# Performance work log

Measured on AMD Instinct MI355X. Metric: run time of the kernel, lower is better.

Reference implementation:

```python
import jax, jax.numpy as jnp
import numpy as np

# ---- static model dims (from init_kwargs) ----
M = 128          # latent_seq_length
Mp1 = M + 1
K = 2 * Mp1      # HMM states (m,g): m in 0..M, g in {0: match, 1: insert}; k = m + (M+1)*g
D = 21           # alphabet_length
ZD = 64          # z_dim
B = 64           # batch size
L = 256          # obs_seq_length
P = Mp1 * 3 * 2  # flattened indel-parameter count (M+1, 3, 2)
NEG = -1e32      # -1/epsilon (pyro Profile epsilon=1e-32) -> forbidden transitions


def _cell_factors(n0, g, mp, gp):
    """Indel log-prob factors (param indices (m,j,s)) for a transition into state (mp,gp)
    when the next undecided ancestral slot is n0 and source type is j=g.
    j: 0=from match, 1=from insert, 2=after deletion. s: 0=no indel, 1=indel.
    Returns (insert_factors, delete_factors) or None if the transition is forbidden."""
    if mp < n0:
        return None
    rs, us = [], []
    if mp == n0:
        if gp == 0:
            rs.append((n0, g, 0)); us.append((n0, g, 0))
        else:
            rs.append((n0, g, 1))
    else:
        rs.append((n0, g, 0)); us.append((n0, g, 1))
        for mm in range(n0 + 1, mp):
            rs.append((mm, 2, 0)); us.append((mm, 2, 1))
        if gp == 0:
            rs.append((mp, 2, 0)); us.append((mp, 2, 0))
        else:
            rs.append((mp, 2, 1))
    return rs, us


def _build_tables():
    k_of = lambda m, g: m + Mp1 * g
    p_of = lambda m, j, s: (m * 3 + j) * 2 + s
    # initial-distribution transfer (dense, small): virtual source (m,g)=(-1,0) -> n0=0
    r0 = np.zeros((P, K), np.float32)
    u0 = np.zeros((P, K), np.float32)
    null0 = np.zeros((K,), np.float32)
    for mp in range(Mp1):
        for gp in range(2):
            f = _cell_factors(0, 0, mp, gp)
            kp = k_of(mp, gp)
            if f is None:
                null0[kp] = 1.0
            else:
                for t in f[0]:
                    r0[p_of(*t), kp] += 1.0
                for t in f[1]:
                    u0[p_of(*t), kp] += 1.0
    # transition-matrix transfer: sparse (param_idx, cell_idx) scatter-add lists
    r_par, r_cell, u_par, u_cell = [], [], [], []
    null = np.zeros((K, K), np.float32)
    for m in range(Mp1):
        for g in range(2):
            n0, k = m + 1 - g, k_of(m, g)
            for mp in range(Mp1):
                for gp in range(2):
                    kp = k_of(mp, gp)
                    f = _cell_factors(n0, g, mp, gp)
                    if f is None:
                        null[k, kp] = 1.0
                    else:
                        cell = k * K + kp
                        for t in f[0]:
                            r_par.append(p_of(*t)); r_cell.append(cell)
                        for t in f[1]:
                            u_par.append(p_of(*t)); u_cell.append(cell)
    return (jnp.asarray(r0), jnp.asarray(u0), jnp.asarray(null0), jnp.asarray(null),
            jnp.asarray(np.asarray(r_par, np.int32)), jnp.asarray(np.asarray(r_cell, np.int32)),
            jnp.asarray(np.asarray(u_par, np.int32)), jnp.asarray(np.asarray(u_cell, np.int32)))


R0, U0, NULL0, NULL, R_PAR, R_CELL, U_PAR, U_CELL = _build_tables()


def setup_inputs() -> dict:
    key = jax.random.key(0)
    ks = jax.random.split(key, 8)
    # variable-length one-hot sequences; missing steps are all-zero rows (pyro convention)
    tokens = jax.random.randint(ks[0], (B, L), 0, D)
    lengths = jax.random.randint(ks[1], (B,), L // 2, L + 1)
    mask = jnp.arange(L)[None, :] < lengths[:, None]
    data = jax.nn.one_hot(tokens, D, dtype=jnp.float32) * mask[:, :, None]
    z = jax.random.normal(ks[2], (B, ZD), jnp.float32)
    out_dim = 2 * Mp1 * D
    dec_W = jax.random.normal(ks[3], (out_dim, ZD), jnp.float32) / np.sqrt(ZD).astype(np.float32)
    dec_b = jax.random.normal(ks[4], (out_dim,), jnp.float32) * 0.01
    indel_prior = jnp.array([10.0, 0.0], jnp.float32)  # [strength, 0]
    insert = indel_prior + jax.random.normal(ks[5], (Mp1, 3, 2), jnp.float32)
    delete = indel_prior + jax.random.normal(ks[6], (Mp1, 3, 2), jnp.float32)
    inverse_temp = 1.0 + 0.1 * jax.random.normal(ks[7], (1,), jnp.float32)
    return {"data": data, "z": z, "dec_W": dec_W, "dec_b": dec_b,
            "insert": insert, "delete": delete, "inverse_temp": inverse_temp}


def reference(data, z, dec_W, dec_b, insert, delete, inverse_temp):
    # ---- Decoder + temperature-sharpened emission logits (FactorMuE.model) ----
    latent = (z @ dec_W.T + dec_b).reshape(-1, 2, Mp1, D)        # (B, 2, M+1, D)
    it = jax.nn.softplus(inverse_temp[0])
    anc = latent[:, 0] * it
    anc = anc - jax.nn.logsumexp(anc, axis=-1, keepdims=True)    # ancestor_seq_logits
    insq = latent[:, 1] * it
    insq = insq - jax.nn.logsumexp(insq, axis=-1, keepdims=True)  # insert_seq_logits
    ilog = insert - jax.nn.logsumexp(insert, axis=-1, keepdims=True)
    dlog = delete - jax.nn.logsumexp(delete, axis=-1, keepdims=True)
    # ---- Profile state arranger: profile-HMM -> dense HMM logits ----
    pi, pd = ilog.reshape(-1), dlog.reshape(-1)                  # (P,)
    a0 = pd @ U0 + pi @ R0 + NEG * NULL0                         # (K,) initial logits
    a = (jnp.zeros((K * K,), pi.dtype)
         .at[U_CELL].add(pd[U_PAR])
         .at[R_CELL].add(pi[R_PAR])).reshape(K, K) + NEG * NULL  # (K, K) transition logits
    e = jnp.concatenate([anc, insq], axis=1)                     # (B, K, D), k = m + (M+1)*g
    # ---- VariableLengthDiscreteHMM (MissingDataDiscreteHMM) log_prob ----
    a0 = a0 - jax.nn.logsumexp(a0)
    a = a - jax.nn.logsumexp(a, axis=-1, keepdims=True)
    e = e - jax.nn.logsumexp(e, axis=-1, keepdims=True)
    vl = jnp.einsum('bld,bkd->lbk', data, e)                     # (L, B, K); zero rows -> 0 (missing)
    alpha = a0 + vl[0]                                           # (B, K)

    def step(alpha, v):
        alpha = jax.nn.logsumexp(alpha[:, :, None] + a[None], axis=1) + v
        return alpha, None

    alpha, _ = jax.lax.scan(step, alpha, vl[1:])
    return jax.nn.logsumexp(alpha, axis=-1)                      # (B,) log-likelihood per sequence
```

## Files before the change

### kernel.cpp

```cpp
#include <hip/hip_runtime.h>
#include <math.h>

#define MP1 129
#define KK  258
#define DD  21
#define ZDIM 64
#define BB  64
#define LL  256

#define OFF_ETG  0
#define OFF_E2G  360448
#define OFF_TOK  363264
#define OFF_COEF 379648
#define C_UU   0
#define C_DXM  258
#define C_DXI  516
#define C_WM   774
#define C_WI   903
#define C_DMID 1032
#define C_PI0  1160

#define EMIS_BLKS 65
#define TOK_BLKS  1366

typedef float f32x2 __attribute__((ext_vector_type(2)));

template <int CTRL, int RM, int BM>
__device__ __forceinline__ float updpp(float old, float src) {
    return __int_as_float(__builtin_amdgcn_update_dpp(
        __float_as_int(old), __float_as_int(src), CTRL, RM, BM, false));
}
__device__ __forceinline__ float readlane_f(float v, int lane) {
    return __int_as_float(__builtin_amdgcn_readlane(__float_as_int(v), lane));
}
__device__ __forceinline__ float wave_sum_to63(float s) {
    s += updpp<0x111, 0xf, 0xf>(0.f, s);
    s += updpp<0x112, 0xf, 0xf>(0.f, s);
    s += updpp<0x114, 0xf, 0xf>(0.f, s);
    s += updpp<0x118, 0xf, 0xf>(0.f, s);
    s += updpp<0x142, 0xa, 0xf>(0.f, s);
    s += updpp<0x143, 0xc, 0xf>(0.f, s);
    return s;
}

__global__ __launch_bounds__(256, 1) void k_setup(const float* __restrict__ z,
                                                  const float* __restrict__ W,
                                                  const float* __restrict__ bias,
                                                  const float* __restrict__ invt,
                                                  const float* __restrict__ data,
                                                  const float* __restrict__ ins,
                                                  const float* __restrict__ del,
                                                  float* __restrict__ ETg,
                                                  float* __restrict__ E2g,
                                                  int* __restrict__ tokout,
                                                  float* __restrict__ coef) {
    __shared__ float il[774], dl[774], Smid[129], Qs[130];
    int bid = blockIdx.x;
    int tid = threadIdx.x;

    if (bid >= 1 && bid <= EMIS_BLKS) {
        int b  = tid & 63;
        int rr = __builtin_amdgcn_readfirstlane((bid - 1) * 4 + (tid >> 6));
        if (rr >= KK) return;
        float it = log1pf(expf(invt[0]));
        const float* wb = W + (size_t)rr * DD * ZDIM;
        const float* bp = bias + rr * DD;
        float acc[DD];
        #pragma unroll
        for (int d = 0; d < DD; ++d) acc[d] = bp[d];
        const float4* zp = (const float4*)(z + (size_t)b * ZDIM);
        #pragma unroll
        for (int c = 0; c < 4; ++c) {
            float4 za = zp[4 * c + 0], zb = zp[4 * c + 1];
            float4 zc = zp[4 * c + 2], zd = zp[4 * c + 3];
            #pragma unroll
            for (int d = 0; d < DD; ++d) {
                const float4* wp = (const float4*)(wb + (size_t)d * ZDIM + 16 * c);
                float4 wa = wp[0], wv = wp[1], wc = wp[2], wd = wp[3];
                float a = acc[d];
                a = fmaf(za.x, wa.x, a); a = fmaf(za.y, wa.y, a);
                a = fmaf(za.z, wa.z, a); a = fmaf(za.w, wa.w, a);
                a = fmaf(zb.x, wv.x, a); a = fmaf(zb.y, wv.y, a);
                a = fmaf(zb.z, wv.z, a); a = fmaf(zb.w, wv.w, a);
                a = fmaf(zc.x, wc.x, a); a = fmaf(zc.y, wc.y, a);
                a = fmaf(zc.z, wc.z, a); a = fmaf(zc.w, wc.w, a);
                a = fmaf(zd.x, wd.x, a); a = fmaf(zd.y, wd.y, a);
                a = fmaf(zd.z, wd.z, a); a = fmaf(zd.w, wd.w, a);
                acc[d] = a;
            }
        }
        float mx = acc[0] * it;
        #pragma unroll
        for (int d = 0; d < DD; ++d) { acc[d] *= it; mx = fmaxf(mx, acc[d]); }
        float s = 0.f;
        #pragma unroll
        for (int d = 0; d < DD; ++d) { acc[d] = expf(acc[d] - mx); s += acc[d]; }
        float inv = 1.0f / s;
        if (rr == 128 || rr == 257) {
            float* eb = E2g + b * 44 + ((rr == 128) ? 0 : 1);
            #pragma unroll
            for (int d = 0; d < DD; ++d) eb[d * 2] = acc[d] * inv;
            eb[DD * 2] = 1.0f;
        } else {
            bool ism = rr < 128;
            int m = ism ? rr : rr - MP1;
            int slot = (m >> 1) * 4 + (ism ? 0 : 2) + (m & 1);
            float* eb = ETg + (size_t)b * 5632 + slot;
            #pragma unroll
            for (int d = 0; d < DD; ++d) eb[d * 256] = acc[d] * inv;
            eb[DD * 256] = 1.0f;
        }
        return;
    }
    if (bid > EMIS_BLKS) {
        int wid  = (bid - 1 - EMIS_BLKS) * 4 + (tid >> 6);
        int lane = tid & 63;
        int r3   = lane / 21;
        int d    = lane - r3 * 21;
        int row  = wid * 3 + r3;
        float v = 0.f;
        if (r3 < 3 && row < BB * LL) v = data[(size_t)row * DD + d];
        unsigned long long m = __ballot(v > 0.5f);
        if (r3 < 3 && d == 0 && row < BB * LL) {
            unsigned long long slice = (m >> (21 * r3)) & 0x1FFFFFULL;
            tokout[row] = slice ? (int)__builtin_ctzll(slice) : DD;
        }
        return;
    }
    int t = tid;
    for (int p = t; p < 387; p += 256) {
        float x0 = ins[2 * p], x1 = ins[2 * p + 1];
        float mx = fmaxf(x0, x1);
        float ls = mx + logf(expf(x0 - mx) + expf(x1 - mx));
        il[2 * p] = x0 - ls; il[2 * p + 1] = x1 - ls;
        float y0 = del[2 * p], y1 = del[2 * p + 1];
        float my = fmaxf(y0, y1);
        float lt = my + logf(expf(y0 - my) + expf(y1 - my));
        dl[2 * p] = y0 - lt; dl[2 * p + 1] = y1 - lt;
    }
    __syncthreads();
    if (t < 64) {
        int mmA = 1 + 2 * t, mmB = 2 + 2 * t;
        float xA = il[(mmA * 3 + 2) * 2 + 0] + dl[(mmA * 3 + 2) * 2 + 1];
        float xB = il[(mmB * 3 + 2) * 2 + 0] + dl[(mmB * 3 + 2) * 2 + 1];
        float sc = xA + xB;
        #pragma unroll
        for (int off = 1; off < 64; off <<= 1) {
            float vv = __shfl_up(sc, off);
            if (t >= off) sc += vv;
        }
        Smid[mmB] = sc;
        Smid[mmA] = sc - xB;
        if (t == 0) Smid[0] = 0.f;
    }
    __syncthreads();
    if (t < 64) {
        int mpA = 128 - 2 * t, mpB = 127 - 2 * t;
        float aM_ = il[(mpA * 3 + 2) * 2 + 0] + dl[(mpA * 3 + 2) * 2 + 0];
        float aI_ = il[(mpA * 3 + 2) * 2 + 1];
        float mA = fmaxf(aM_, aI_);
        float pA = Smid[mpA - 1] + mA + logf(expf(aM_ - mA) + expf(aI_ - mA));
        float bM_ = il[(mpB * 3 + 2) * 2 + 0] + dl[(mpB * 3 + 2) * 2 + 0];
        float bI_ = il[(mpB * 3 + 2) * 2 + 1];
        float mB = fmaxf(bM_, bI_);
        float pB = Smid[mpB - 1] + mB + logf(expf(bM_ - mB) + expf(bI_ - mB));
        float cm = fmaxf(pA, pB);
        float cs = expf(pA - cm) + expf(pB - cm);
        #pragma unroll
        for (int off = 1; off < 64; off <<= 1) {
            float om = __shfl_up(cm, off);
            float os = __shfl_up(cs, off);
            if (t >= off) {
                float M = fmaxf(cm, om);
                cs = cs * expf(cm - M) + os * expf(om - M);
                cm = M;
            }
        }
        Qs[mpB] = cm + logf(cs);
        float em = __shfl_up(cm, 1), es = __shfl_up(cs, 1);
        if (t == 0) Qs[128] = pA;
        else {
            float M = fmaxf(em, pA);
            Qs[mpA] = M + logf(es * expf(em - M) + expf(pA - M));
        }
        if (t == 0) Qs[129] = -1e30f;
    }
    __syncthreads();
    float* uu  = coef + C_UU;
    float* dxM = coef + C_DXM;
    float* dxI = coef + C_DXI;
    float* wM  = coef + C_WM;
    float* wI  = coef + C_WI;
    float* dmd = coef + C_DMID;
    float* pi0 = coef + C_PI0;
    for (int k = t; k < KK; k += 256) {
        if (k == 128) { uu[k] = 0.f; dxM[k] = 0.f; dxI[k] = 0.f; continue; }
        int g  = (k < MP1) ? 0 : 1;
        int n0 = g ? (k - MP1) : (k + 1);
        float i0 = il[(n0 * 3 + g) * 2 + 0], i1 = il[(n0 * 3 + g) * 2 + 1];
        float e0 = dl[(n0 * 3 + g) * 2 + 0], e1 = dl[(n0 * 3 + g) * 2 + 1];
        float diagM = i0 + e0;
        float diagI = i1;
        float src   = i0 + e1;
        float tail  = src - Smid[n0] + Qs[n0 + 1];
        float M3 = fmaxf(fmaxf(diagM, diagI), tail);
        float ssum = expf(diagM - M3) + expf(diagI - M3) + expf(tail - M3);
        float lse = M3 + logf(ssum);
        uu[k]  = expf(src - lse);
        dxM[k] = expf(diagM - lse);
        dxI[k] = expf(diagI - lse);
    }
    for (int mp = t; mp < MP1; mp += 256) {
        wM[mp] = expf(il[(mp * 3 + 2) * 2 + 0] + dl[(mp * 3 + 2) * 2 + 0]);
        wI[mp] = expf(il[(mp * 3 + 2) * 2 + 1]);
    }
    for (int tt = t; tt < 128; tt += 256)
        dmd[tt] = (tt == 0) ? 1.f : expf(il[(tt * 3 + 2) * 2 + 0] + dl[(tt * 3 + 2) * 2 + 1]);
    __syncthreads();
    {
        float i00 = il[0], i01 = il[1], d00 = dl[0], d01 = dl[1];
        float a00 = i00 + d00, a0129 = i01;
        float tail0 = i00 + d01 + Qs[1];
        float M3 = fmaxf(fmaxf(a00, a0129), tail0);
        float lse0 = M3 + logf(expf(a00 - M3) + expf(a0129 - M3) + expf(tail0 - M3));
        for (int kp = t; kp < KK; kp += 256) {
            int gp = (kp >= MP1);
            int mp = gp ? (kp - MP1) : kp;
            float v;
            if (mp == 0) v = gp ? a0129 : a00;
            else v = i00 + d01 + Smid[mp - 1] +
                     (gp ? il[(mp * 3 + 2) * 2 + 1]
                         : il[(mp * 3 + 2) * 2 + 0] + dl[(mp * 3 + 2) * 2 + 0]);
            pi0[kp] = expf(v - lse0);
        }
    }
}

__global__ __launch_bounds__(64) void k_fwd(const float* __restrict__ ETg,
                                            const float* __restrict__ E2g,
                                            const int* __restrict__ tokg,
                                            const float* __restrict__ coef,
                                            float* __restrict__ out) {
    const float* uu  = coef + C_UU;
    const float* dxM = coef + C_DXM;
    const float* dxI = coef + C_DXI;
    const float* wMg = coef + C_WM;
    const float* wIg = coef + C_WI;
    const float* dmd = coef + C_DMID;
    const float* pi0 = coef + C_PI0;
    __shared__ float ETLs[22 * 256];
    int lane = threadIdx.x;
    int b = blockIdx.x;
    const float4* srcp = (const float4*)(ETg + (size_t)b * 5632);
    float4* dstp = (float4*)ETLs;
    for (int i = lane; i < 1408; i += 64) dstp[i] = srcp[i];
    float e2m = 0.f, e2i = 0.f;
    if (lane < 22) {
        e2m = E2g[b * 44 + lane * 2 + 0];
        e2i = E2g[b * 44 + lane * 2 + 1];
    }
    int4 tkv = ((const int4*)(tokg + b * LL))[lane];
    __syncthreads();

    int m0 = 2 * lane, m1 = 2 * lane + 1;
    bool L0 = (lane == 0), L63 = (lane == 63);
    float f63 = L63 ? 1.f : 0.f;
    float cM0 = L0 ? 0.f : uu[m0 - 1];
    float cM1 = uu[m0];
    f32x2 cIp  = {uu[129 + m0], uu[129 + m1]};
    float d0 = dmd[m0], d1v = dmd[m1];
    float Apair = d0 * d1v;
    f32x2 wMp  = {wMg[m0], wMg[m1]};
    f32x2 wIp  = {wIg[m0], wIg[m1]};
    f32x2 xMAp = {L0 ? 0.f : dxM[m0 - 1], dxM[m0]};
    f32x2 xIAp = {L0 ? 0.f : dxI[m0 - 1], dxI[m0]};
    f32x2 xMBp = {dxM[129 + m0], dxM[129 + m1]};
    f32x2 xIBp = {dxI[129 + m0], dxI[129 + m1]};
    f32x2 w2p  = {L63 ? wMg[128] : 0.f, L63 ? wIg[128] : 0.f};
    f32x2 xA2p = {L63 ? dxM[127] : 0.f, L63 ? dxI[127] : 0.f};
    f32x2 xB2p = {L63 ? dxM[257] : 0.f, L63 ? dxI[257] : 0.f};
    f32x2 f63p = {f63, f63};

    float A0 = Apair;
    float A1 = A0 * updpp<0x111, 0xf, 0xf>(1.f, A0);
    float A2 = A1 * updpp<0x112, 0xf, 0xf>(1.f, A1);
    float A3 = A2 * updpp<0x114, 0xf, 0xf>(1.f, A2);
    float A4 = A3 * updpp<0x118, 0xf, 0xf>(1.f, A3);
    float A5 = A4 * updpp<0x142, 0xa, 0xf>(1.f, A4);
    unsigned long long bbf = __ballot(Apair >= 1.0e-3f);
    int fast = (bbf == 0ULL);

    int lidx = lane * 4;
    int tok0 = __builtin_amdgcn_readlane(tkv.x, 0);
    float4 q0 = *(const float4*)(ETLs + tok0 * 256 + lidx);
    f32x2 e20 = {readlane_f(e2m, tok0), readlane_f(e2i, tok0)};
    f32x2 aM = {pi0[m0] * q0.x, pi0[m1] * q0.y};
    f32x2 aI = {pi0[129 + m0] * q0.z, pi0[129 + m1] * q0.w};
    f32x2 a2 = {f63 * pi0[128] * e20.x, f63 * pi0[257] * e20.y};

    int etot = 0;
    f32x2 part = (aM + aI) + a2;

    float4 q1, q2, q3, q4;
    int st1, st2, st3, st4;
#define LOADR(QN, SN, TN)                                                    \
    { int tn_ = (TN); SN = tn_;                                              \
      QN = *(const float4*)(ETLs + tn_ * 256 + lidx); }
    LOADR(q1, st1, __builtin_amdgcn_readlane(tkv.y, 0));
    LOADR(q2, st2, __builtin_amdgcn_readlane(tkv.z, 0));
    LOADR(q3, st3, __builtin_amdgcn_readlane(tkv.w, 0));
    LOADR(q4, st4, __builtin_amdgcn_readlane(tkv.x, 1));

#define STEP_BODY(RES, PART, NL, Qr, STr)                                    \
    {                                                                        \
        f32x2 EMv = {Qr.x, Qr.y};                                            \
        f32x2 EIv = {Qr.z, Qr.w};                                            \
        f32x2 E2v = {readlane_f(e2m, STr), readlane_f(e2i, STr)};            \
        if (RES) {                                                           \
            float s_ = wave_sum_to63(part.x + part.y);                       \
            float stot = readlane_f(s_, 63);                                 \
            int sb = __float_as_int(stot) & 0x7f800000;                      \
            etot += (sb >> 23);                                              \
            float invs = __int_as_float(0x7f000000 - sb);                    \
            f32x2 iv = {invs, invs};                                         \
            EMv *= iv; EIv *= iv; E2v *= iv;                                 \
        }                                                                    \
        float aMp  = updpp<0x138, 0xf, 0xf>(0.f, aM.y);        \
        float u128 = readlane_f(a2.x, 63);                                   \
        f32x2 aIc = aI * cIp;                                                \
        float r0 = fmaf(aMp, cM0, aIc.x);                                    \
        float r1 = fmaf(aM.x, cM1, aIc.y);                                   \
        float B = fmaf(d1v, r0, r1);                                         \
        B = fmaf(A0, updpp<0x111, 0xf, 0xf>(0.f, B), B);                     \
        if (NL > 1) {                                                        \
            B = fmaf(A1, updpp<0x112, 0xf, 0xf>(0.f, B), B);                 \
            B = fmaf(A2, updpp<0x114, 0xf, 0xf>(0.f, B), B);                 \
            B = fmaf(A3, updpp<0x118, 0xf, 0xf>(0.f, B), B);                 \
            B = fmaf(A4, updpp<0x142, 0xa, 0xf>(0.f, B), B);                 \
            B = fmaf(A5, updpp<0x143, 0xc, 0xf>(0.f, B), B);                 \
        }                                                                    \
        float G0 = updpp<0x138, 0xf, 0xf>(0.f, B);                           \
        float G1 = fmaf(d0, G0, r0);                                         \
        f32x2 Gp   = {G0, G1};                                               \
        f32x2 aMs  = {aMp, aM.x};                                            \
        f32x2 u2   = {u128, u128};                                           \
        f32x2 G2p  = {B, B};                                                 \
        f32x2 aM1s = {aM.y, aM.y};                                           \
        f32x2 aI2s = {a2.y, a2.y};                                           \
        f32x2 mM = wMp * Gp + (xMAp * aMs + (xMBp * aI + u2));               \
        f32x2 mI = wIp * Gp + (xIAp * aMs + (xIBp * aI + u2));               \
        f32x2 m2 = w2p * G2p + (xA2p * aM1s + (xB2p * aI2s + u2));           \
        aM = mM * EMv;                                                       \
        aI = mI * EIv;                                                       \
        a2 = m2 * E2v * f63p;                                                \
        if (PART) part = (aM + aI) + a2;                                     \
    }

#define RUN_SCAN(NL)                                                         \
    for (int it = 0; it < 63; ++it) {                                        \
        STEP_BODY(1, 0, NL, q1, st1);                                        \
        LOADR(q1, st1, __builtin_amdgcn_readlane(tkv.y, it + 1));            \
        STEP_BODY(0, 0, NL, q2, st2);                                        \
        LOADR(q2, st2, __builtin_amdgcn_readlane(tkv.z, it + 1));            \
        STEP_BODY(0, 0, NL, q3, st3);                                        \
        LOADR(q3, st3, __builtin_amdgcn_readlane(tkv.w, it + 1));            \
        STEP_BODY(0, 1, NL, q4, st4);                                        \
        int it2 = (it + 2 < 64) ? (it + 2) : 63;                             \
        LOADR(q4, st4, __builtin_amdgcn_readlane(tkv.x, it2));               \
    }                                                                        \
    STEP_BODY(1, 0, NL, q1, st1);                                            \
    STEP_BODY(0, 0, NL, q2, st2);                                            \
    STEP_BODY(0, 1, NL, q3, st3);

    if (fast) { RUN_SCAN(1) }
    else      { RUN_SCAN(6) }
#undef RUN_SCAN
#undef STEP_BODY
#undef LOADR

    float s = wave_sum_to63(part.x + part.y);
    if (lane == 63)
        out[b] = (float)(etot - 64 * 127) * 0.6931471805599453f + logf(s);
}

extern "C" void kernel_launch(void* const* d_in, const int* in_sizes, int n_in,
                              void* d_out, int out_size, void* d_ws, size_t ws_size,
                              hipStream_t stream) {
    const float* data  = (const float*)d_in[0];
    const float* z     = (const float*)d_in[1];
    const float* dec_W = (const float*)d_in[2];
    const float* dec_b = (const float*)d_in[3];
    const float* ins   = (const float*)d_in[4];
    const float* del   = (const float*)d_in[5];
    const float* invt  = (const float*)d_in[6];
    float* out = (float*)d_out;

    float* ws   = (float*)d_ws;
    float* ETg  = ws + OFF_ETG;
    float* E2g  = ws + OFF_E2G;
    int*   tok  = (int*)(ws + OFF_TOK);
    float* coef = ws + OFF_COEF;

    k_setup<<<1 + EMIS_BLKS + TOK_BLKS, 256, 0, stream>>>(z, dec_W, dec_b, invt,
                                                          data, ins, del, ETg, E2g,
                                                          tok, coef);
    k_fwd<<<BB, 64, 0, stream>>>(ETg, E2g, tok, coef, out);
}
```

Baseline: 49.37 us.

## Unroll scan to eight steps per iteration, renormalize every eight, add zero-carry fast path

The forward-scan loop is unrolled from four to eight timesteps per iteration, with twice as many prefetched emission rows in flight, and rescaling now happens every eight steps instead of every four. The fast path now applies when every lane except lane 0 has a pair product below 1e-8, and it drops the carry prefix scan completely (NL=0) instead of keeping one DPP stage. This cuts reduction and DPP work per step, but risks float underflow over eight unnormalized steps and approximates away small deletion-chain terms. The output exponent correction is changed to match the halved number of renormalizations.

```diff
diff --git a/kernel.cpp b/kernel.cpp
--- a/kernel.cpp
+++ b/kernel.cpp
@@ -287,8 +287,8 @@
     float A3 = A2 * updpp<0x114, 0xf, 0xf>(1.f, A2);
     float A4 = A3 * updpp<0x118, 0xf, 0xf>(1.f, A3);
     float A5 = A4 * updpp<0x142, 0xa, 0xf>(1.f, A4);
-    unsigned long long bbf = __ballot(Apair >= 1.0e-3f);
-    int fast = (bbf == 0ULL);
+    unsigned long long bb0 = __ballot(Apair >= 1.0e-8f) & ~1ULL;
+    int fast0 = (bb0 == 0ULL);
 
     int lidx = lane * 4;
     int tok0 = __builtin_amdgcn_readlane(tkv.x, 0);
@@ -301,8 +301,8 @@
     int etot = 0;
     f32x2 part = (aM + aI) + a2;
 
-    float4 q1, q2, q3, q4;
-    int st1, st2, st3, st4;
+    float4 q1, q2, q3, q4, q5, q6, q7, q8;
+    int st1, st2, st3, st4, st5, st6, st7, st8;
 #define LOADR(QN, SN, TN)                                                    \
     { int tn_ = (TN); SN = tn_;                                              \
       QN = *(const float4*)(ETLs + tn_ * 256 + lidx); }
@@ -310,6 +310,10 @@
     LOADR(q2, st2, __builtin_amdgcn_readlane(tkv.z, 0));
     LOADR(q3, st3, __builtin_amdgcn_readlane(tkv.w, 0));
     LOADR(q4, st4, __builtin_amdgcn_readlane(tkv.x, 1));
+    LOADR(q5, st5, __builtin_amdgcn_readlane(tkv.y, 1));
+    LOADR(q6, st6, __builtin_amdgcn_readlane(tkv.z, 1));
+    LOADR(q7, st7, __builtin_amdgcn_readlane(tkv.w, 1));
+    LOADR(q8, st8, __builtin_amdgcn_readlane(tkv.x, 2));
 
 #define STEP_BODY(RES, PART, NL, Qr, STr)                                    \
     {                                                                        \
@@ -331,8 +335,8 @@
         float r0 = fmaf(aMp, cM0, aIc.x);                                    \
         float r1 = fmaf(aM.x, cM1, aIc.y);                                   \
         float B = fmaf(d1v, r0, r1);                                         \
-        B = fmaf(A0, updpp<0x111, 0xf, 0xf>(0.f, B), B);                     \
-        if (NL > 1) {                                                        \
+        if (NL > 0) {                                                        \
+            B = fmaf(A0, updpp<0x111, 0xf, 0xf>(0.f, B), B);                 \
             B = fmaf(A1, updpp<0x112, 0xf, 0xf>(0.f, B), B);                 \
             B = fmaf(A2, updpp<0x114, 0xf, 0xf>(0.f, B), B);                 \
             B = fmaf(A3, updpp<0x118, 0xf, 0xf>(0.f, B), B);                 \
@@ -357,30 +361,44 @@
     }
 
 #define RUN_SCAN(NL)                                                         \
-    for (int it = 0; it < 63; ++it) {                                        \
+    for (int g = 0; g < 31; ++g) {                                           \
+        int lg = 2 * g;                                                      \
         STEP_BODY(1, 0, NL, q1, st1);                                        \
-        LOADR(q1, st1, __builtin_amdgcn_readlane(tkv.y, it + 1));            \
+        LOADR(q1, st1, __builtin_amdgcn_readlane(tkv.y, lg + 2));            \
         STEP_BODY(0, 0, NL, q2, st2);                                        \
-        LOADR(q2, st2, __builtin_amdgcn_readlane(tkv.z, it + 1));            \
+        LOADR(q2, st2, __builtin_amdgcn_readlane(tkv.z, lg + 2));            \
         STEP_BODY(0, 0, NL, q3, st3);                                        \
-        LOADR(q3, st3, __builtin_amdgcn_readlane(tkv.w, it + 1));            \
-        STEP_BODY(0, 1, NL, q4, st4);                                        \
-        int it2 = (it + 2 < 64) ? (it + 2) : 63;                             \
-        LOADR(q4, st4, __builtin_amdgcn_readlane(tkv.x, it2));               \
+        LOADR(q3, st3, __builtin_amdgcn_readlane(tkv.w, lg + 2));            \
+        STEP_BODY(0, 0, NL, q4, st4);                                        \
+        LOADR(q4, st4, __builtin_amdgcn_readlane(tkv.x, lg + 3));            \
+        STEP_BODY(0, 0, NL, q5, st5);                                        \
+        LOADR(q5, st5, __builtin_amdgcn_readlane(tkv.y, lg + 3));            \
+        STEP_BODY(0, 0, NL, q6, st6);                                        \
+        LOADR(q6, st6, __builtin_amdgcn_readlane(tkv.z, lg + 3));            \
+        STEP_BODY(0, 0, NL, q7, st7);                                        \
+        LOADR(q7, st7, __builtin_amdgcn_readlane(tkv.w, lg + 3));            \
+        STEP_BODY(0, 1, NL, q8, st8);                                        \
+        int lc = (lg + 4 < 64) ? (lg + 4) : 63;                              \
+        LOADR(q8, st8, __builtin_amdgcn_readlane(tkv.x, lc));                \
     }                                                                        \
+                     \
     STEP_BODY(1, 0, NL, q1, st1);                                            \
     STEP_BODY(0, 0, NL, q2, st2);                                            \
-    STEP_BODY(0, 1, NL, q3, st3);
-
-    if (fast) { RUN_SCAN(1) }
-    else      { RUN_SCAN(6) }
+    STEP_BODY(0, 0, NL, q3, st3);                                            \
+    STEP_BODY(0, 0, NL, q4, st4);                                            \
+    STEP_BODY(0, 0, NL, q5, st5);                                            \
+    STEP_BODY(0, 0, NL, q6, st6);                                            \
+    STEP_BODY(0, 1, NL, q7, st7);
+
+    if (fast0) { RUN_SCAN(0) }
+    else       { RUN_SCAN(6) }
 #undef RUN_SCAN
 #undef STEP_BODY
 #undef LOADR
 
     float s = wave_sum_to63(part.x + part.y);
     if (lane == 63)
-        out[b] = (float)(etot - 64 * 127) * 0.6931471805599453f + logf(s);
+        out[b] = (float)(etot - 32 * 127) * 0.6931471805599453f + logf(s);
 }
 
 extern "C" void kernel_launch(void* const* d_in, const int* in_sizes, int n_in,
```

Result: slower. 54.07 us (+9.5%).

## Fuse setup and forward kernels into one per-batch block kernel

Applied to the files above, without the earlier changes.

Merges the setup kernel (emission softmax, token extraction, indel coefficient prep) and the forward recursion kernel into a single launch of 64 blocks, one per batch item. Emissions, tokens and coefficients now go into shared memory instead of a global workspace. This removes one kernel launch and the global round trip, but every block recomputes the shared indel coefficients, and only 64 blocks do the emission GEMV, with each thread handling about one state row serially. The token scan also changes from a wave ballot to a per-thread loop over 21 elements.

```diff
diff --git a/kernel.cpp b/kernel.cpp
--- a/kernel.cpp
+++ b/kernel.cpp
@@ -8,10 +8,6 @@
 #define BB  64
 #define LL  256
 
-#define OFF_ETG  0
-#define OFF_E2G  360448
-#define OFF_TOK  363264
-#define OFF_COEF 379648
 #define C_UU   0
 #define C_DXM  258
 #define C_DXI  516
@@ -19,9 +15,6 @@
 #define C_WI   903
 #define C_DMID 1032
 #define C_PI0  1160
-
-#define EMIS_BLKS 65
-#define TOK_BLKS  1366
 
 typedef float f32x2 __attribute__((ext_vector_type(2)));
 
@@ -43,92 +36,82 @@
     return s;
 }
 
-__global__ __launch_bounds__(256, 1) void k_setup(const float* __restrict__ z,
+__global__ __launch_bounds__(256, 1) void k_fused(const float* __restrict__ z,
                                                   const float* __restrict__ W,
                                                   const float* __restrict__ bias,
                                                   const float* __restrict__ invt,
                                                   const float* __restrict__ data,
                                                   const float* __restrict__ ins,
                                                   const float* __restrict__ del,
-                                                  float* __restrict__ ETg,
-                                                  float* __restrict__ E2g,
-                                                  int* __restrict__ tokout,
-                                                  float* __restrict__ coef) {
+                                                  float* __restrict__ out) {
+    __shared__ __align__(16) float ETLs[22 * 256];
+    __shared__ float E2L[22 * 2];
+    __shared__ __align__(16) int tokL[LL];
     __shared__ float il[774], dl[774], Smid[129], Qs[130];
-    int bid = blockIdx.x;
+    __shared__ float cf[1418];
     int tid = threadIdx.x;
-
-    if (bid >= 1 && bid <= EMIS_BLKS) {
-        int b  = tid & 63;
-        int rr = __builtin_amdgcn_readfirstlane((bid - 1) * 4 + (tid >> 6));
-        if (rr >= KK) return;
+    int b   = blockIdx.x;
+
+    {
+        const float* r = data + ((size_t)b * LL + tid) * DD;
+        int idx = DD; float ssum = 0.f;
+        for (int d = 0; d < DD; ++d) { float v = r[d]; ssum += v; if (v > 0.5f) idx = d; }
+        tokL[tid] = (ssum > 0.5f) ? idx : DD;
+    }
+
+    {
         float it = log1pf(expf(invt[0]));
-        const float* wb = W + (size_t)rr * DD * ZDIM;
-        const float* bp = bias + rr * DD;
-        float acc[DD];
-        #pragma unroll
-        for (int d = 0; d < DD; ++d) acc[d] = bp[d];
         const float4* zp = (const float4*)(z + (size_t)b * ZDIM);
-        #pragma unroll
-        for (int c = 0; c < 4; ++c) {
-            float4 za = zp[4 * c + 0], zb = zp[4 * c + 1];
-            float4 zc = zp[4 * c + 2], zd = zp[4 * c + 3];
+        for (int rr = tid; rr < KK; rr += 256) {
+            const float* wb = W + (size_t)rr * DD * ZDIM;
+            const float* bp = bias + rr * DD;
+            float acc[DD];
             #pragma unroll
-            for (int d = 0; d < DD; ++d) {
-                const float4* wp = (const float4*)(wb + (size_t)d * ZDIM + 16 * c);
-                float4 wa = wp[0], wv = wp[1], wc = wp[2], wd = wp[3];
-                float a = acc[d];
-                a = fmaf(za.x, wa.x, a); a = fmaf(za.y, wa.y, a);
-                a = fmaf(za.z, wa.z, a); a = fmaf(za.w, wa.w, a);
-                a = fmaf(zb.x, wv.x, a); a = fmaf(zb.y, wv.y, a);
-                a = fmaf(zb.z, wv.z, a); a = fmaf(zb.w, wv.w, a);
-                a = fmaf(zc.x, wc.x, a); a = fmaf(zc.y, wc.y, a);
-                a = fmaf(zc.z, wc.z, a); a = fmaf(zc.w, wc.w, a);
-                a = fmaf(zd.x, wd.x, a); a = fmaf(zd.y, wd.y, a);
-                a = fmaf(zd.z, wd.z, a); a = fmaf(zd.w, wd.w, a);
-                acc[d] = a;
+            for (int d = 0; d < DD; ++d) acc[d] = bp[d];
+            #pragma unroll
+            for (int c = 0; c < 4; ++c) {
+                float4 za = zp[4 * c + 0], zb = zp[4 * c + 1];
+                float4 zc = zp[4 * c + 2], zd = zp[4 * c + 3];
+                #pragma unroll
+                for (int d = 0; d < DD; ++d) {
+                    const float4* wp = (const float4*)(wb + (size_t)d * ZDIM + 16 * c);
+                    float4 wa = wp[0], wv = wp[1], wc = wp[2], wd = wp[3];
+                    float a = acc[d];
+                    a = fmaf(za.x, wa.x, a); a = fmaf(za.y, wa.y, a);
+                    a = fmaf(za.z, wa.z, a); a = fmaf(za.w, wa.w, a);
+                    a = fmaf(zb.x, wv.x, a); a = fmaf(zb.y, wv.y, a);
+                    a = fmaf(zb.z, wv.z, a); a = fmaf(zb.w, wv.w, a);
+                    a = fmaf(zc.x, wc.x, a); a = fmaf(zc.y, wc.y, a);
+                    a = fmaf(zc.z, wc.z, a); a = fmaf(zc.w, wc.w, a);
+                    a = fmaf(zd.x, wd.x, a); a = fmaf(zd.y, wd.y, a);
+                    a = fmaf(zd.z, wd.z, a); a = fmaf(zd.w, wd.w, a);
+                    acc[d] = a;
+                }
             }
-        }
-        float mx = acc[0] * it;
-        #pragma unroll
-        for (int d = 0; d < DD; ++d) { acc[d] *= it; mx = fmaxf(mx, acc[d]); }
-        float s = 0.f;
-        #pragma unroll
-        for (int d = 0; d < DD; ++d) { acc[d] = expf(acc[d] - mx); s += acc[d]; }
-        float inv = 1.0f / s;
-        if (rr == 128 || rr == 257) {
-            float* eb = E2g + b * 44 + ((rr == 128) ? 0 : 1);
+            float mx = acc[0] * it;
             #pragma unroll
-            for (int d = 0; d < DD; ++d) eb[d * 2] = acc[d] * inv;
-            eb[DD * 2] = 1.0f;
-        } else {
-            bool ism = rr < 128;
-            int m = ism ? rr : rr - MP1;
-            int slot = (m >> 1) * 4 + (ism ? 0 : 2) + (m & 1);
-            float* eb = ETg + (size_t)b * 5632 + slot;
+            for (int d = 0; d < DD; ++d) { acc[d] *= it; mx = fmaxf(mx, acc[d]); }
+            float s = 0.f;
             #pragma unroll
-            for (int d = 0; d < DD; ++d) eb[d * 256] = acc[d] * inv;
-            eb[DD * 256] = 1.0f;
-        }
-        return;
-    }
-    if (bid > EMIS_BLKS) {
-        int wid  = (bid - 1 - EMIS_BLKS) * 4 + (tid >> 6);
-        int lane = tid & 63;
-        int r3   = lane / 21;
-        int d    = lane - r3 * 21;
-        int row  = wid * 3 + r3;
-        float v = 0.f;
-        if (r3 < 3 && row < BB * LL) v = data[(size_t)row * DD + d];
-        unsigned long long m = __ballot(v > 0.5f);
-        if (r3 < 3 && d == 0 && row < BB * LL) {
-            unsigned long long slice = (m >> (21 * r3)) & 0x1FFFFFULL;
-            tokout[row] = slice ? (int)__builtin_ctzll(slice) : DD;
-        }
-        return;
-    }
-    int t = tid;
-    for (int p = t; p < 387; p += 256) {
+            for (int d = 0; d < DD; ++d) { acc[d] = expf(acc[d] - mx); s += acc[d]; }
+            float inv = 1.0f / s;
+            if (rr == 128 || rr == 257) {
+                float* eb = E2L + ((rr == 128) ? 0 : 1);
+                #pragma unroll
+                for (int d = 0; d < DD; ++d) eb[d * 2] = acc[d] * inv;
+                eb[DD * 2] = 1.0f;
+            } else {
+                bool ism = rr < 128;
+                int m = ism ? rr : rr - MP1;
+                int slot = (m >> 1) * 4 + (ism ? 0 : 2) + (m & 1);
+                #pragma unroll
+                for (int d = 0; d < DD; ++d) ETLs[d * 256 + slot] = acc[d] * inv;
+                ETLs[DD * 256 + slot] = 1.0f;
+            }
+        }
+    }
+
+    for (int p = tid; p < 387; p += 256) {
         float x0 = ins[2 * p], x1 = ins[2 * p + 1];
         float mx = fmaxf(x0, x1);
         float ls = mx + logf(expf(x0 - mx) + expf(x1 - mx));
@@ -139,23 +122,23 @@
         dl[2 * p] = y0 - lt; dl[2 * p + 1] = y1 - lt;
     }
     __syncthreads();
-    if (t < 64) {
-        int mmA = 1 + 2 * t, mmB = 2 + 2 * t;
+    if (tid < 64) {
+        int mmA = 1 + 2 * tid, mmB = 2 + 2 * tid;
         float xA = il[(mmA * 3 + 2) * 2 + 0] + dl[(mmA * 3 + 2) * 2 + 1];
         float xB = il[(mmB * 3 + 2) * 2 + 0] + dl[(mmB * 3 + 2) * 2 + 1];
         float sc = xA + xB;
         #pragma unroll
         for (int off = 1; off < 64; off <<= 1) {
             float vv = __shfl_up(sc, off);
-            if (t >= off) sc += vv;
+            if (tid >= off) sc += vv;
         }
         Smid[mmB] = sc;
         Smid[mmA] = sc - xB;
-        if (t == 0) Smid[0] = 0.f;
+        if (tid == 0) Smid[0] = 0.f;
     }
     __syncthreads();
-    if (t < 64) {
-        int mpA = 128 - 2 * t, mpB = 127 - 2 * t;
+    if (tid < 64) {
+        int mpA = 128 - 2 * tid, mpB = 127 - 2 * tid;
         float aM_ = il[(mpA * 3 + 2) * 2 + 0] + dl[(mpA * 3 + 2) * 2 + 0];
         float aI_ = il[(mpA * 3 + 2) * 2 + 1];
         float mA = fmaxf(aM_, aI_);
@@ -170,7 +153,7 @@
         for (int off = 1; off < 64; off <<= 1) {
             float om = __shfl_up(cm, off);
             float os = __shfl_up(cs, off);
-            if (t >= off) {
+            if (tid >= off) {
                 float M = fmaxf(cm, om);
                 cs = cs * expf(cm - M) + os * expf(om - M);
                 cm = M;
@@ -178,52 +161,51 @@
         }
         Qs[mpB] = cm + logf(cs);
         float em = __shfl_up(cm, 1), es = __shfl_up(cs, 1);
-        if (t == 0) Qs[128] = pA;
+        if (tid == 0) Qs[128] = pA;
         else {
             float M = fmaxf(em, pA);
             Qs[mpA] = M + logf(es * expf(em - M) + expf(pA - M));
         }
-        if (t == 0) Qs[129] = -1e30f;
-    }
-    __syncthreads();
-    float* uu  = coef + C_UU;
-    float* dxM = coef + C_DXM;
-    float* dxI = coef + C_DXI;
-    float* wM  = coef + C_WM;
-    float* wI  = coef + C_WI;
-    float* dmd = coef + C_DMID;
-    float* pi0 = coef + C_PI0;
-    for (int k = t; k < KK; k += 256) {
-        if (k == 128) { uu[k] = 0.f; dxM[k] = 0.f; dxI[k] = 0.f; continue; }
-        int g  = (k < MP1) ? 0 : 1;
-        int n0 = g ? (k - MP1) : (k + 1);
-        float i0 = il[(n0 * 3 + g) * 2 + 0], i1 = il[(n0 * 3 + g) * 2 + 1];
-        float e0 = dl[(n0 * 3 + g) * 2 + 0], e1 = dl[(n0 * 3 + g) * 2 + 1];
-        float diagM = i0 + e0;
-        float diagI = i1;
-        float src   = i0 + e1;
-        float tail  = src - Smid[n0] + Qs[n0 + 1];
-        float M3 = fmaxf(fmaxf(diagM, diagI), tail);
-        float ssum = expf(diagM - M3) + expf(diagI - M3) + expf(tail - M3);
-        float lse = M3 + logf(ssum);
-        uu[k]  = expf(src - lse);
-        dxM[k] = expf(diagM - lse);
-        dxI[k] = expf(diagI - lse);
-    }
-    for (int mp = t; mp < MP1; mp += 256) {
-        wM[mp] = expf(il[(mp * 3 + 2) * 2 + 0] + dl[(mp * 3 + 2) * 2 + 0]);
-        wI[mp] = expf(il[(mp * 3 + 2) * 2 + 1]);
-    }
-    for (int tt = t; tt < 128; tt += 256)
-        dmd[tt] = (tt == 0) ? 1.f : expf(il[(tt * 3 + 2) * 2 + 0] + dl[(tt * 3 + 2) * 2 + 1]);
+        if (tid == 0) Qs[129] = -1e30f;
+    }
     __syncthreads();
     {
+        float* uu  = cf + C_UU;
+        float* dxM = cf + C_DXM;
+        float* dxI = cf + C_DXI;
+        float* wM  = cf + C_WM;
+        float* wI  = cf + C_WI;
+        float* dmd = cf + C_DMID;
+        float* pi0 = cf + C_PI0;
+        for (int k = tid; k < KK; k += 256) {
+            if (k == 128) { uu[k] = 0.f; dxM[k] = 0.f; dxI[k] = 0.f; continue; }
+            int g  = (k < MP1) ? 0 : 1;
+            int n0 = g ? (k - MP1) : (k + 1);
+            float i0 = il[(n0 * 3 + g) * 2 + 0], i1 = il[(n0 * 3 + g) * 2 + 1];
+            float e0 = dl[(n0 * 3 + g) * 2 + 0], e1 = dl[(n0 * 3 + g) * 2 + 1];
+            float diagM = i0 + e0;
+            float diagI = i1;
+            float src   = i0 + e1;
+            float tail  = src - Smid[n0] + Qs[n0 + 1];
+            float M3 = fmaxf(fmaxf(diagM, diagI), tail);
+            float ssum = expf(diagM - M3) + expf(diagI - M3) + expf(tail - M3);
+            float lse = M3 + logf(ssum);
+            uu[k]  = expf(src - lse);
+            dxM[k] = expf(diagM - lse);
+            dxI[k] = expf(diagI - lse);
+        }
+        for (int mp = tid; mp < MP1; mp += 256) {
+            wM[mp] = expf(il[(mp * 3 + 2) * 2 + 0] + dl[(mp * 3 + 2) * 2 + 0]);
+            wI[mp] = expf(il[(mp * 3 + 2) * 2 + 1]);
+        }
+        for (int tt = tid; tt < 128; tt += 256)
+            dmd[tt] = (tt == 0) ? 1.f : expf(il[(tt * 3 + 2) * 2 + 0] + dl[(tt * 3 + 2) * 2 + 1]);
         float i00 = il[0], i01 = il[1], d00 = dl[0], d01 = dl[1];
         float a00 = i00 + d00, a0129 = i01;
         float tail0 = i00 + d01 + Qs[1];
         float M3 = fmaxf(fmaxf(a00, a0129), tail0);
         float lse0 = M3 + logf(expf(a00 - M3) + expf(a0129 - M3) + expf(tail0 - M3));
-        for (int kp = t; kp < KK; kp += 256) {
+        for (int kp = tid; kp < KK; kp += 256) {
             int gp = (kp >= MP1);
             int mp = gp ? (kp - MP1) : kp;
             float v;
@@ -234,33 +216,23 @@
             pi0[kp] = expf(v - lse0);
         }
     }
-}
-
-__global__ __launch_bounds__(64) void k_fwd(const float* __restrict__ ETg,
-                                            const float* __restrict__ E2g,
-                                            const int* __restrict__ tokg,
-                                            const float* __restrict__ coef,
-                                            float* __restrict__ out) {
-    const float* uu  = coef + C_UU;
-    const float* dxM = coef + C_DXM;
-    const float* dxI = coef + C_DXI;
-    const float* wMg = coef + C_WM;
-    const float* wIg = coef + C_WI;
-    const float* dmd = coef + C_DMID;
-    const float* pi0 = coef + C_PI0;
-    __shared__ float ETLs[22 * 256];
-    int lane = threadIdx.x;
-    int b = blockIdx.x;
-    const float4* srcp = (const float4*)(ETg + (size_t)b * 5632);
-    float4* dstp = (float4*)ETLs;
-    for (int i = lane; i < 1408; i += 64) dstp[i] = srcp[i];
+    __syncthreads();
+
+    if (tid >= 64) return;
+    const float* uu  = cf + C_UU;
+    const float* dxM = cf + C_DXM;
+    const float* dxI = cf + C_DXI;
+    const float* wMg = cf + C_WM;
+    const float* wIg = cf + C_WI;
+    const float* dmd = cf + C_DMID;
+    const float* pi0 = cf + C_PI0;
+    int lane = tid;
     float e2m = 0.f, e2i = 0.f;
     if (lane < 22) {
-        e2m = E2g[b * 44 + lane * 2 + 0];
-        e2i = E2g[b * 44 + lane * 2 + 1];
-    }
-    int4 tkv = ((const int4*)(tokg + b * LL))[lane];
-    __syncthreads();
+        e2m = E2L[lane * 2 + 0];
+        e2i = E2L[lane * 2 + 1];
+    }
+    int4 tkv = ((const int4*)tokL)[lane];
 
     int m0 = 2 * lane, m1 = 2 * lane + 1;
     bool L0 = (lane == 0), L63 = (lane == 63);
@@ -394,15 +366,7 @@
     const float* del   = (const float*)d_in[5];
     const float* invt  = (const float*)d_in[6];
     float* out = (float*)d_out;
-
-    float* ws   = (float*)d_ws;
-    float* ETg  = ws + OFF_ETG;
-    float* E2g  = ws + OFF_E2G;
-    int*   tok  = (int*)(ws + OFF_TOK);
-    float* coef = ws + OFF_COEF;
-
-    k_setup<<<1 + EMIS_BLKS + TOK_BLKS, 256, 0, stream>>>(z, dec_W, dec_b, invt,
-                                                          data, ins, del, ETg, E2g,
-                                                          tok, coef);
-    k_fwd<<<BB, 64, 0, stream>>>(ETg, E2g, tok, coef, out);
-}
+    (void)d_ws; (void)ws_size;
+
+    k_fused<<<BB, 256, 0, stream>>>(z, dec_W, dec_b, invt, data, ins, del, out);
+}
```

Result: slower. 75.65 us (+53.2%).

## Pre-gather per-position emission rows into a dense buffer before forward scan

Applied to the files above, without the earlier changes.

Adds a k_gather kernel that uses the tokens to copy each sequence position's emission row (and the extra-state emissions) into a dense (B, L, 256) global buffer. The forward kernel then streams these rows sequentially from global memory. This drops the LDS staging, the token reads via readlane and the per-step readlane of the extra-state emissions. The cost is an extra kernel launch, a 16 MB write/read round trip, and global-memory latency inside the serial scan, where the old version read from LDS.

```diff
diff --git a/kernel.cpp b/kernel.cpp
--- a/kernel.cpp
+++ b/kernel.cpp
@@ -8,10 +8,12 @@
 #define BB  64
 #define LL  256
 
-#define OFF_ETG  0
-#define OFF_E2G  360448
-#define OFF_TOK  363264
-#define OFF_COEF 379648
+#define OFF_ETT  0
+#define OFF_E2T  4194304
+#define OFF_ETG  4227072
+#define OFF_E2G  4587520
+#define OFF_TOK  4590336
+#define OFF_COEF 4606720
 #define C_UU   0
 #define C_DXM  258
 #define C_DXI  516
@@ -236,9 +238,25 @@
     }
 }
 
-__global__ __launch_bounds__(64) void k_fwd(const float* __restrict__ ETg,
-                                            const float* __restrict__ E2g,
-                                            const int* __restrict__ tokg,
+__global__ __launch_bounds__(256) void k_gather(const float* __restrict__ ETg,
+                                                const float* __restrict__ E2g,
+                                                const int* __restrict__ tok,
+                                                float* __restrict__ ETt,
+                                                float* __restrict__ E2t) {
+    int wid  = blockIdx.x * 4 + (threadIdx.x >> 6);
+    int lane = threadIdx.x & 63;
+    int t = __builtin_amdgcn_readfirstlane(tok[wid]);
+    int b = wid >> 8;
+    float4 v = *(const float4*)(ETg + (size_t)b * 5632 + t * 256 + lane * 4);
+    *(float4*)(ETt + (size_t)wid * 256 + lane * 4) = v;
+    if (lane == 0) {
+        E2t[wid * 2 + 0] = E2g[b * 44 + t * 2 + 0];
+        E2t[wid * 2 + 1] = E2g[b * 44 + t * 2 + 1];
+    }
+}
+
+__global__ __launch_bounds__(64) void k_fwd(const float* __restrict__ ETt,
+                                            const float* __restrict__ E2t,
                                             const float* __restrict__ coef,
                                             float* __restrict__ out) {
     const float* uu  = coef + C_UU;
@@ -248,19 +266,10 @@
     const float* wIg = coef + C_WI;
     const float* dmd = coef + C_DMID;
     const float* pi0 = coef + C_PI0;
-    __shared__ float ETLs[22 * 256];
     int lane = threadIdx.x;
     int b = blockIdx.x;
-    const float4* srcp = (const float4*)(ETg + (size_t)b * 5632);
-    float4* dstp = (float4*)ETLs;
-    for (int i = lane; i < 1408; i += 64) dstp[i] = srcp[i];
-    float e2m = 0.f, e2i = 0.f;
-    if (lane < 22) {
-        e2m = E2g[b * 44 + lane * 2 + 0];
-        e2i = E2g[b * 44 + lane * 2 + 1];
-    }
-    int4 tkv = ((const int4*)(tokg + b * LL))[lane];
-    __syncthreads();
+    const float* etb = ETt + (size_t)b * LL * 256;
+    const float* e2b = E2t + (size_t)b * LL * 2;
 
     int m0 = 2 * lane, m1 = 2 * lane + 1;
     bool L0 = (lane == 0), L63 = (lane == 63);
@@ -290,10 +299,8 @@
     unsigned long long bbf = __ballot(Apair >= 1.0e-3f);
     int fast = (bbf == 0ULL);
 
-    int lidx = lane * 4;
-    int tok0 = __builtin_amdgcn_readlane(tkv.x, 0);
-    float4 q0 = *(const float4*)(ETLs + tok0 * 256 + lidx);
-    f32x2 e20 = {readlane_f(e2m, tok0), readlane_f(e2i, tok0)};
+    float4 q0 = *((const float4*)etb + lane);
+    f32x2 e20 = *(const f32x2*)e2b;
     f32x2 aM = {pi0[m0] * q0.x, pi0[m1] * q0.y};
     f32x2 aI = {pi0[129 + m0] * q0.z, pi0[129 + m1] * q0.w};
     f32x2 a2 = {f63 * pi0[128] * e20.x, f63 * pi0[257] * e20.y};
@@ -301,21 +308,22 @@
     int etot = 0;
     f32x2 part = (aM + aI) + a2;
 
+    const float4* pq = (const float4*)(etb + 256) + lane;
+    const f32x2* pe = (const f32x2*)e2b + 1;
     float4 q1, q2, q3, q4;
-    int st1, st2, st3, st4;
-#define LOADR(QN, SN, TN)                                                    \
-    { int tn_ = (TN); SN = tn_;                                              \
-      QN = *(const float4*)(ETLs + tn_ * 256 + lidx); }
-    LOADR(q1, st1, __builtin_amdgcn_readlane(tkv.y, 0));
-    LOADR(q2, st2, __builtin_amdgcn_readlane(tkv.z, 0));
-    LOADR(q3, st3, __builtin_amdgcn_readlane(tkv.w, 0));
-    LOADR(q4, st4, __builtin_amdgcn_readlane(tkv.x, 1));
-
-#define STEP_BODY(RES, PART, NL, Qr, STr)                                    \
+    f32x2 e21, e22, e23, e24;
+#define LOADR(QN, EN)                                                        \
+    { QN = *pq; pq += 64; EN = *pe; pe += 1; }
+    LOADR(q1, e21);
+    LOADR(q2, e22);
+    LOADR(q3, e23);
+    LOADR(q4, e24);
+
+#define STEP_BODY(RES, PART, NL, Qr, E2r)                                    \
     {                                                                        \
         f32x2 EMv = {Qr.x, Qr.y};                                            \
         f32x2 EIv = {Qr.z, Qr.w};                                            \
-        f32x2 E2v = {readlane_f(e2m, STr), readlane_f(e2i, STr)};            \
+        f32x2 E2v = E2r;                                                     \
         if (RES) {                                                           \
             float s_ = wave_sum_to63(part.x + part.y);                       \
             float stot = readlane_f(s_, 63);                                 \
@@ -358,19 +366,18 @@
 
 #define RUN_SCAN(NL)                                                         \
     for (int it = 0; it < 63; ++it) {                                        \
-        STEP_BODY(1, 0, NL, q1, st1);                                        \
-        LOADR(q1, st1, __builtin_amdgcn_readlane(tkv.y, it + 1));            \
-        STEP_BODY(0, 0, NL, q2, st2);                                        \
-        LOADR(q2, st2, __builtin_amdgcn_readlane(tkv.z, it + 1));            \
-        STEP_BODY(0, 0, NL, q3, st3);                                        \
-        LOADR(q3, st3, __builtin_amdgcn_readlane(tkv.w, it + 1));            \
-        STEP_BODY(0, 1, NL, q4, st4);                                        \
-        int it2 = (it + 2 < 64) ? (it + 2) : 63;                             \
-        LOADR(q4, st4, __builtin_amdgcn_readlane(tkv.x, it2));               \
+        STEP_BODY(1, 0, NL, q1, e21);                                        \
+        LOADR(q1, e21);                                                      \
+        STEP_BODY(0, 0, NL, q2, e22);                                        \
+        LOADR(q2, e22);                                                      \
+        STEP_BODY(0, 0, NL, q3, e23);                                        \
+        LOADR(q3, e23);                                                      \
+        STEP_BODY(0, 1, NL, q4, e24);                                        \
+        LOADR(q4, e24);                                                      \
     }                                                                        \
-    STEP_BODY(1, 0, NL, q1, st1);                                            \
-    STEP_BODY(0, 0, NL, q2, st2);                                            \
-    STEP_BODY(0, 1, NL, q3, st3);
+    STEP_BODY(1, 0, NL, q1, e21);                                            \
+    STEP_BODY(0, 0, NL, q2, e22);                                            \
+    STEP_BODY(0, 1, NL, q3, e23);
 
     if (fast) { RUN_SCAN(1) }
     else      { RUN_SCAN(6) }
@@ -396,6 +403,8 @@
     float* out = (float*)d_out;
 
     float* ws   = (float*)d_ws;
+    float* ETt  = ws + OFF_ETT;
+    float* E2t  = ws + OFF_E2T;
     float* ETg  = ws + OFF_ETG;
     float* E2g  = ws + OFF_E2G;
     int*   tok  = (int*)(ws + OFF_TOK);
@@ -404,5 +413,6 @@
     k_setup<<<1 + EMIS_BLKS + TOK_BLKS, 256, 0, stream>>>(z, dec_W, dec_b, invt,
                                                           data, ins, del, ETg, E2g,
                                                           tok, coef);
-    k_fwd<<<BB, 64, 0, stream>>>(ETg, E2g, tok, coef, out);
-}
+    k_gather<<<BB * LL / 4, 256, 0, stream>>>(ETg, E2g, tok, ETt, E2t);
+    k_fwd<<<BB, 64, 0, stream>>>(ETt, E2t, coef, out);
+}
```

New measurement: 65.50 us. +32.7%, slower.
